# Performance work log

Measured on AMD Instinct MI355X. Metric: run time of the kernel, lower is better.

Reference implementation:

```python
import jax, jax.numpy as jnp
import numpy as np

B, S, D, H = 4, 2048, 1024, 16
DH = D // H  # 64


def setup_inputs() -> dict:
    key = jax.random.key(0)
    ks = jax.random.split(key, 8)
    sc = 1.0 / np.sqrt(D)
    return {
        "hidden_states": jax.random.normal(ks[0], (B, S, D), jnp.float32),
        "attention_mask": jnp.zeros((B, 1, 1, S), jnp.float32),
        "Wq": jax.random.normal(ks[1], (D, D), jnp.float32) * sc,
        "bq": jnp.zeros((D,), jnp.float32),
        "Wk": jax.random.normal(ks[2], (D, D), jnp.float32) * sc,
        "bk": jnp.zeros((D,), jnp.float32),
        "Wv": jax.random.normal(ks[3], (D, D), jnp.float32) * sc,
        "bv": jnp.zeros((D,), jnp.float32),
    }


def _heads(x):
    # [B,S,D] -> [B,H,S,DH]
    b, s, _ = x.shape
    return x.reshape(b, s, H, DH).transpose(0, 2, 1, 3)


def reference(hidden_states, attention_mask, Wq, bq, Wk, bk, Wv, bv):
    q = _heads(hidden_states @ Wq + bq)
    k = _heads(hidden_states @ Wk + bk)
    v = _heads(hidden_states @ Wv + bv)
    scores = jnp.einsum('bhqd,bhkd->bhqk', q, k) / jnp.sqrt(jnp.float32(DH))
    scores = scores + attention_mask  # additive mask, broadcast
    probs = jax.nn.softmax(scores, axis=-1)  # dropout is identity in eval
    out = jnp.einsum('bhqk,bhkd->bhqd', probs, v)
    b, h, s, dh = out.shape
    return out.transpose(0, 2, 1, 3).reshape(b, s, h * dh)
```

## Files before the change

kernel.cpp:

```cpp
#include <hip/hip_runtime.h>
#include <hip/hip_bf16.h>
#include <cstdint>

typedef _Float16 f16;
typedef f16 f16x8 __attribute__((ext_vector_type(8)));
typedef f16 f16x4 __attribute__((ext_vector_type(4)));
typedef float f32x4 __attribute__((ext_vector_type(4)));

#define MFMA16(a, b, c) __builtin_amdgcn_mfma_f32_16x16x32_f16((a), (b), (c), 0, 0, 0)

constexpr int Bc = 4, Sc = 2048, Dc = 1024, Hc = 16, DHc = 64;

typedef __attribute__((address_space(1))) const uint32_t gbl_u32;
typedef __attribute__((address_space(3))) uint32_t lds_u32;
__device__ __forceinline__ void gld_lds16(const void* g, void* l) {
  __builtin_amdgcn_global_load_lds((gbl_u32*)g, (lds_u32*)l, 16, 0, 0);
}

__global__ __launch_bounds__(256) void cast_w_kernel(
    const float* __restrict__ Wq, const float* __restrict__ Wk,
    const float* __restrict__ Wv, f16* __restrict__ Wt) {
  __shared__ __align__(16) f16 T[64][66];
  const int z = blockIdx.z;
  const float* W = (z == 0) ? Wq : (z == 1) ? Wk : Wv;
  const int n0 = blockIdx.x * 64, k0 = blockIdx.y * 64;
  const int t = threadIdx.x;
#pragma unroll
  for (int p = 0; p < 4; p++) {
    int idx = t + p * 256;
    int r = idx >> 4, c = idx & 15;
    float4 v = *(const float4*)(W + (size_t)(k0 + r) * Dc + n0 + c * 4);
    T[r][c * 4 + 0] = (f16)v.x;
    T[r][c * 4 + 1] = (f16)v.y;
    T[r][c * 4 + 2] = (f16)v.z;
    T[r][c * 4 + 3] = (f16)v.w;
  }
  __syncthreads();
#pragma unroll
  for (int p = 0; p < 2; p++) {
    int idx = t + p * 256;
    int n = idx >> 3, c = idx & 7;
    f16x8 tmp;
#pragma unroll
    for (int j = 0; j < 8; j++) tmp[j] = T[c * 8 + j][n];
    *(f16x8*)(Wt + ((size_t)z * Dc + n0 + n) * Dc + k0 + c * 8) = tmp;
  }
}

__global__ __launch_bounds__(256) void cast_x_kernel(const float* __restrict__ X,
                                                     f16* __restrict__ X16) {
  size_t i = ((size_t)blockIdx.x * 256 + threadIdx.x) * 8;
  float4 a = *(const float4*)(X + i);
  float4 b = *(const float4*)(X + i + 4);
  f16x8 h;
  h[0] = (f16)a.x; h[1] = (f16)a.y; h[2] = (f16)a.z; h[3] = (f16)a.w;
  h[4] = (f16)b.x; h[5] = (f16)b.y; h[6] = (f16)b.z; h[7] = (f16)b.w;
  *(f16x8*)(X16 + i) = h;
}

__global__ __launch_bounds__(256) void qkv_gemm_kernel(
    const f16* __restrict__ X16, const f16* __restrict__ Wt,
    const float* __restrict__ bq, const float* __restrict__ bk,
    const float* __restrict__ bv, f16* __restrict__ Qo, f16* __restrict__ Ko,
    f16* __restrict__ Vo) {
  const int lin = blockIdx.x;
  const int xcd = lin & 7, jj = lin >> 3;
  const int bn = jj >> 3;
  const int bm = (xcd << 3) | (jj & 7);
  const int z = bn >> 3;
  const int n0 = (bn & 7) * 128;
  const int m0 = bm * 128;
  const f16* W = Wt + (size_t)bn * 128 * Dc;
  const float* bias = (z == 0) ? bq : (z == 1) ? bk : bv;

  __shared__ __align__(16) f16 Xs[128 * 32];
  __shared__ __align__(16) f16 Ws[128 * 32];

  const int t = threadIdx.x;
  const int wave = t >> 6, lane = t & 63;
  const int l16 = lane & 15, quad = lane >> 4;
  const int wm = (wave >> 1) * 64, wn = (wave & 1) * 64;

  f32x4 acc[4][4];
#pragma unroll
  for (int i = 0; i < 4; i++)
#pragma unroll
    for (int j = 0; j < 4; j++) acc[i][j] = (f32x4){0.f, 0.f, 0.f, 0.f};

  for (int k0 = 0; k0 < Dc; k0 += 32) {
#pragma unroll
    for (int p = 0; p < 2; p++) {
      int cb = p * 256 + wave * 64;
      int chunk = cb + lane;
      int row = chunk >> 2, c8 = (chunk & 3) * 8;
      gld_lds16(X16 + (size_t)(m0 + row) * Dc + k0 + c8, (f16*)Xs + (size_t)cb * 8);
      gld_lds16(W + (size_t)row * Dc + k0 + c8, (f16*)Ws + (size_t)cb * 8);
    }
    __syncthreads();

    f16x8 aF[4], bF[4];
#pragma unroll
    for (int mt = 0; mt < 4; mt++)
      aF[mt] = *(const f16x8*)(&Xs[(wm + mt * 16 + l16) * 32 + quad * 8]);
#pragma unroll
    for (int nt = 0; nt < 4; nt++)
      bF[nt] = *(const f16x8*)(&Ws[(wn + nt * 16 + l16) * 32 + quad * 8]);
#pragma unroll
    for (int mt = 0; mt < 4; mt++)
#pragma unroll
      for (int nt = 0; nt < 4; nt++)
        acc[mt][nt] = MFMA16(aF[mt], bF[nt], acc[mt][nt]);
    __syncthreads();
  }

#pragma unroll
  for (int nt = 0; nt < 4; nt++) {
    int col = n0 + wn + nt * 16 + l16;
    float bval = bias[col];
    int h = col >> 6, d = col & 63;
    if (z == 2) {
#pragma unroll
      for (int mt = 0; mt < 4; mt++) {
        int m = m0 + wm + mt * 16 + quad * 4;
        int b = m >> 11, sbase = m & 2047;
        f16x4 pk;
#pragma unroll
        for (int r = 0; r < 4; r++) pk[r] = (f16)(acc[mt][nt][r] + bval);
        *(f16x4*)(Vo + (((size_t)(b * Hc + h)) * DHc + d) * Sc + sbase) = pk;
      }
    } else {
      const float sc = (z == 0) ? 0.18033688011112042f : 1.0f;
      f16* O = (z == 0) ? Qo : Ko;
#pragma unroll
      for (int mt = 0; mt < 4; mt++) {
#pragma unroll
        for (int r = 0; r < 4; r++) {
          int m = m0 + wm + mt * 16 + quad * 4 + r;
          int b = m >> 11, s = m & 2047;
          O[(((size_t)(b * Hc + h)) * Sc + s) * DHc + d] =
              (f16)((acc[mt][nt][r] + bval) * sc);
        }
      }
    }
  }
}

__global__ __launch_bounds__(256) void flash_kernel(
    const f16* __restrict__ Q, const f16* __restrict__ K,
    const f16* __restrict__ Vt, const float* __restrict__ mask,
    float* __restrict__ out) {
  const int lin = blockIdx.x;
  const int xcd = lin & 7, jj = lin >> 3;
  const int bh = (xcd << 3) | (jj & 7);
  const int qt = jj >> 3;
  const int b = bh >> 4, h = bh & 15;
  const int t = threadIdx.x;
  const int wave = t >> 6, lane = t & 63;
  const int l16 = lane & 15, quad = lane >> 4;
  const int qbase = qt * 128 + wave * 32;

  __shared__ __align__(16) f16 Ks[2][4096];
  __shared__ __align__(16) f16 Vs[2][4096];
  __shared__ __align__(16) float Ms[2048];

  const f16* Kb = K + (size_t)bh * Sc * DHc;
  const f16* Vb = Vt + (size_t)bh * DHc * Sc;

  constexpr float L2E = 1.44269504088896340736f;

  const int qsw8 = (quad ^ ((l16 >> 1) & 3)) * 8;

  const f16* kp[2];
  const f16* vp[2];
  int ldsOff[2];
#pragma unroll
  for (int p = 0; p < 2; p++) {
    int cb = p * 256 + wave * 64;
    int i = cb + lane;
    int half = i >> 8, row = (i >> 2) & 63, q8 = i & 3;
    int q8g = q8 ^ ((row >> 1) & 3);
    int g = (row & 32) | ((row & 12) << 1) | ((row & 16) >> 2) | (row & 3);
    kp[p] = Kb + (size_t)g * DHc + half * 32 + q8g * 8;
    vp[p] = Vb + (size_t)row * Sc + half * 32 + q8g * 8;
    ldsOff[p] = cb * 8;
  }
  auto stage = [&](int buf) {
#pragma unroll
    for (int p = 0; p < 2; p++) {
      gld_lds16(kp[p], (f16*)Ks + buf * 4096 + ldsOff[p]);
      gld_lds16(vp[p], (f16*)Vs + buf * 4096 + ldsOff[p]);
      kp[p] += 64 * DHc;
      vp[p] += 64;
    }
  };

  f16x8 qa[2][2];
#pragma unroll
  for (int mt = 0; mt < 2; mt++) {
    const f16* qb = Q + ((size_t)bh * Sc + qbase + mt * 16 + l16) * DHc;
    qa[mt][0] = *(const f16x8*)(qb + quad * 8);
    qa[mt][1] = *(const f16x8*)(qb + 32 + quad * 8);
  }

  f16x8 ones;
#pragma unroll
  for (int j = 0; j < 8; j++) ones[j] = (f16)1.0f;

  stage(0);
  {
    const float* mrow = mask + (size_t)b * Sc + t * 8;
    float4 a0 = *(const float4*)(mrow);
    float4 a1 = *(const float4*)(mrow + 4);
    f32x4 m0 = (f32x4){a0.x * L2E, a0.y * L2E, a0.z * L2E, a0.w * L2E};
    f32x4 m1 = (f32x4){a1.x * L2E, a1.y * L2E, a1.z * L2E, a1.w * L2E};
    *(f32x4*)(&Ms[t * 8]) = m0;
    *(f32x4*)(&Ms[t * 8 + 4]) = m1;
  }
  __syncthreads();

  f32x4 lacc[2];
  f32x4 o[2][4];
#pragma unroll
  for (int mt = 0; mt < 2; mt++) {
    lacc[mt] = (f32x4){0.f, 0.f, 0.f, 0.f};
#pragma unroll
    for (int dt = 0; dt < 4; dt++) o[mt][dt] = (f32x4){0.f, 0.f, 0.f, 0.f};
  }

  for (int c = 0; c < 32; c++) {
    const int buf = c & 1;
    if (c < 31) stage(buf ^ 1);

    const int mb = c * 64 + quad * 8;
    f32x4 minit[4];
    minit[0] = *(const f32x4*)(&Ms[mb + 0]);
    minit[1] = *(const f32x4*)(&Ms[mb + 4]);
    minit[2] = *(const f32x4*)(&Ms[mb + 32]);
    minit[3] = *(const f32x4*)(&Ms[mb + 36]);

    f16x8 ka[4][2];
#pragma unroll
    for (int nt = 0; nt < 4; nt++) {
      int rb = (nt * 16 + l16) * 32 + qsw8;
      ka[nt][0] = *(const f16x8*)(&Ks[buf][rb]);
      ka[nt][1] = *(const f16x8*)(&Ks[buf][2048 + rb]);
    }

    f32x4 s0[4], s1[4];
#pragma unroll
    for (int nt = 0; nt < 4; nt++) {
      f32x4 a = minit[nt];
      a = MFMA16(ka[nt][0], qa[0][0], a);
      a = MFMA16(ka[nt][1], qa[0][1], a);
      s0[nt] = a;
      f32x4 a2 = minit[nt];
      a2 = MFMA16(ka[nt][0], qa[1][0], a2);
      a2 = MFMA16(ka[nt][1], qa[1][1], a2);
      s1[nt] = a2;
    }

    f16x8 pa[2][2];
#pragma unroll
    for (int blk = 0; blk < 2; blk++) {
      f16x8 p0, p1;
#pragma unroll
      for (int half = 0; half < 2; half++) {
        int nt = blk * 2 + half;
#pragma unroll
        for (int r = 0; r < 4; r++) {
          p0[half * 4 + r] = (f16)__builtin_amdgcn_exp2f(s0[nt][r]);
          p1[half * 4 + r] = (f16)__builtin_amdgcn_exp2f(s1[nt][r]);
        }
      }
      pa[0][blk] = p0;
      pa[1][blk] = p1;
    }

    lacc[0] = MFMA16(pa[0][0], ones, lacc[0]);
    lacc[0] = MFMA16(pa[0][1], ones, lacc[0]);
    lacc[1] = MFMA16(pa[1][0], ones, lacc[1]);
    lacc[1] = MFMA16(pa[1][1], ones, lacc[1]);

#pragma unroll
    for (int dt = 0; dt < 4; dt++) {
      int rb = (dt * 16 + l16) * 32 + qsw8;
      f16x8 v0 = *(const f16x8*)(&Vs[buf][rb]);
      f16x8 v1 = *(const f16x8*)(&Vs[buf][2048 + rb]);
      o[0][dt] = MFMA16(pa[0][0], v0, o[0][dt]);
      o[0][dt] = MFMA16(pa[0][1], v1, o[0][dt]);
      o[1][dt] = MFMA16(pa[1][0], v0, o[1][dt]);
      o[1][dt] = MFMA16(pa[1][1], v1, o[1][dt]);
    }

    __syncthreads();
  }

#pragma unroll
  for (int mt = 0; mt < 2; mt++) {
    float inv[4];
#pragma unroll
    for (int r = 0; r < 4; r++) inv[r] = 1.0f / lacc[mt][r];
#pragma unroll
    for (int dt = 0; dt < 4; dt++) {
      int col = h * 64 + dt * 16 + l16;
#pragma unroll
      for (int r = 0; r < 4; r++) {
        int row = qbase + mt * 16 + quad * 4 + r;
        out[((size_t)b * Sc + row) * Dc + col] = o[mt][dt][r] * inv[r];
      }
    }
  }
}

extern "C" void kernel_launch(void* const* d_in, const int* in_sizes, int n_in,
                              void* d_out, int out_size, void* d_ws,
                              size_t ws_size, hipStream_t stream) {
  (void)in_sizes; (void)n_in; (void)out_size; (void)ws_size;
  const float* hidden = (const float*)d_in[0];
  const float* mask   = (const float*)d_in[1];
  const float* Wq     = (const float*)d_in[2];
  const float* bq     = (const float*)d_in[3];
  const float* Wk     = (const float*)d_in[4];
  const float* bk     = (const float*)d_in[5];
  const float* Wv     = (const float*)d_in[6];
  const float* bv     = (const float*)d_in[7];
  float* out = (float*)d_out;

  uint8_t* w = (uint8_t*)d_ws;
  f16* Wt   = (f16*)(w);
  f16* X16  = (f16*)(w + (size_t)6 * 1024 * 1024);
  f16* Q16  = (f16*)(w + (size_t)22 * 1024 * 1024);
  f16* K16  = (f16*)(w + (size_t)38 * 1024 * 1024);
  f16* Vt16 = (f16*)(w + (size_t)54 * 1024 * 1024);

  cast_w_kernel<<<dim3(16, 16, 3), 256, 0, stream>>>(Wq, Wk, Wv, Wt);
  cast_x_kernel<<<4096, 256, 0, stream>>>(hidden, X16);
  qkv_gemm_kernel<<<dim3(1536), 256, 0, stream>>>(X16, Wt, bq, bk, bv,
                                                  Q16, K16, Vt16);
  flash_kernel<<<dim3(1024), 256, 0, stream>>>(Q16, K16, Vt16, mask, out);
}
```

Baseline: 257.3 us.

## Split QKV GEMM into QK and V kernels with K64 swizzled LDS tiles

The single QKV projection GEMM is split into a Q/K kernel and a separate V kernel, which removes the per-block z-branch in the epilogue. Both kernels raise the K step from 32 to 64 and use an XOR-swizzled LDS layout, which halves the number of barriers per K loop and avoids LDS bank conflicts. The Q/K kernel also swaps MFMA operand order so each lane holds four consecutive head-dim values, which allows vectorized f16x4 stores and float4 bias loads instead of scalar stores. The cost is twice the LDS per block, which may lower occupancy, plus one extra kernel launch.

New measurement: 264.6 us. 2.8% more time.

```diff
diff --git a/kernel.cpp b/kernel.cpp
--- a/kernel.cpp
+++ b/kernel.cpp
@@ -58,11 +58,10 @@
   *(f16x8*)(X16 + i) = h;
 }
 
-__global__ __launch_bounds__(256) void qkv_gemm_kernel(
+__global__ __launch_bounds__(256) void qk_gemm_kernel(
     const f16* __restrict__ X16, const f16* __restrict__ Wt,
     const float* __restrict__ bq, const float* __restrict__ bk,
-    const float* __restrict__ bv, f16* __restrict__ Qo, f16* __restrict__ Ko,
-    f16* __restrict__ Vo) {
+    f16* __restrict__ Qo, f16* __restrict__ Ko) {
   const int lin = blockIdx.x;
   const int xcd = lin & 7, jj = lin >> 3;
   const int bn = jj >> 3;
@@ -71,10 +70,12 @@
   const int n0 = (bn & 7) * 128;
   const int m0 = bm * 128;
   const f16* W = Wt + (size_t)bn * 128 * Dc;
-  const float* bias = (z == 0) ? bq : (z == 1) ? bk : bv;
-
-  __shared__ __align__(16) f16 Xs[128 * 32];
-  __shared__ __align__(16) f16 Ws[128 * 32];
+  const float* bias = (z == 0) ? bq : bk;
+  f16* O = (z == 0) ? Qo : Ko;
+  const float sc = (z == 0) ? 0.18033688011112042f : 1.0f;
+
+  __shared__ __align__(16) f16 Xs[128 * 64];
+  __shared__ __align__(16) f16 Ws[128 * 64];
 
   const int t = threadIdx.x;
   const int wave = t >> 6, lane = t & 63;
@@ -87,60 +88,140 @@
 #pragma unroll
     for (int j = 0; j < 4; j++) acc[i][j] = (f32x4){0.f, 0.f, 0.f, 0.f};
 
-  for (int k0 = 0; k0 < Dc; k0 += 32) {
-#pragma unroll
-    for (int p = 0; p < 2; p++) {
-      int cb = p * 256 + wave * 64;
-      int chunk = cb + lane;
-      int row = chunk >> 2, c8 = (chunk & 3) * 8;
-      gld_lds16(X16 + (size_t)(m0 + row) * Dc + k0 + c8, (f16*)Xs + (size_t)cb * 8);
-      gld_lds16(W + (size_t)row * Dc + k0 + c8, (f16*)Ws + (size_t)cb * 8);
+  for (int k0 = 0; k0 < Dc; k0 += 64) {
+#pragma unroll
+    for (int p = 0; p < 4; p++) {
+      int i = p * 256 + wave * 64 + lane;
+      int row = i >> 3, oct = i & 7;
+      int so = (oct ^ (row & 7)) * 8;
+      gld_lds16(X16 + (size_t)(m0 + row) * Dc + k0 + so, (f16*)Xs + (size_t)i * 8);
+      gld_lds16(W + (size_t)row * Dc + k0 + so, (f16*)Ws + (size_t)i * 8);
     }
     __syncthreads();
 
-    f16x8 aF[4], bF[4];
-#pragma unroll
-    for (int mt = 0; mt < 4; mt++)
-      aF[mt] = *(const f16x8*)(&Xs[(wm + mt * 16 + l16) * 32 + quad * 8]);
-#pragma unroll
-    for (int nt = 0; nt < 4; nt++)
-      bF[nt] = *(const f16x8*)(&Ws[(wn + nt * 16 + l16) * 32 + quad * 8]);
-#pragma unroll
-    for (int mt = 0; mt < 4; mt++)
+    f16x8 aF[4][2], bF[4][2];
+#pragma unroll
+    for (int mt = 0; mt < 4; mt++) {
+      int r = wm + mt * 16 + l16;
+#pragma unroll
+      for (int kk = 0; kk < 2; kk++)
+        aF[mt][kk] =
+            *(const f16x8*)(&Xs[r * 64 + (((kk * 4 + quad) ^ (r & 7)) * 8)]);
+    }
+#pragma unroll
+    for (int nt = 0; nt < 4; nt++) {
+      int r = wn + nt * 16 + l16;
+#pragma unroll
+      for (int kk = 0; kk < 2; kk++)
+        bF[nt][kk] =
+            *(const f16x8*)(&Ws[r * 64 + (((kk * 4 + quad) ^ (r & 7)) * 8)]);
+    }
+#pragma unroll
+    for (int kk = 0; kk < 2; kk++)
 #pragma unroll
       for (int nt = 0; nt < 4; nt++)
-        acc[mt][nt] = MFMA16(aF[mt], bF[nt], acc[mt][nt]);
+#pragma unroll
+        for (int mt = 0; mt < 4; mt++)
+          acc[nt][mt] = MFMA16(bF[nt][kk], aF[mt][kk], acc[nt][mt]);
+    __syncthreads();
+  }
+
+  const int h = (n0 + wn) >> 6;
+#pragma unroll
+  for (int nt = 0; nt < 4; nt++) {
+    int cb = n0 + wn + nt * 16 + quad * 4;
+    float4 bv4 = *(const float4*)(bias + cb);
+    int d0 = nt * 16 + quad * 4;
+#pragma unroll
+    for (int mt = 0; mt < 4; mt++) {
+      int m = m0 + wm + mt * 16 + l16;
+      int b = m >> 11, s = m & 2047;
+      f16x4 pk;
+      pk[0] = (f16)((acc[nt][mt][0] + bv4.x) * sc);
+      pk[1] = (f16)((acc[nt][mt][1] + bv4.y) * sc);
+      pk[2] = (f16)((acc[nt][mt][2] + bv4.z) * sc);
+      pk[3] = (f16)((acc[nt][mt][3] + bv4.w) * sc);
+      *(f16x4*)(O + (((size_t)(b * Hc + h)) * Sc + s) * DHc + d0) = pk;
+    }
+  }
+}
+
+__global__ __launch_bounds__(256) void v_gemm_kernel(
+    const f16* __restrict__ X16, const f16* __restrict__ Wt,
+    const float* __restrict__ bv, f16* __restrict__ Vo) {
+  const int lin = blockIdx.x;
+  const int xcd = lin & 7, jj = lin >> 3;
+  const int bn = jj >> 3;
+  const int bm = (xcd << 3) | (jj & 7);
+  const int n0 = bn * 128;
+  const int m0 = bm * 128;
+  const f16* W = Wt + ((size_t)2048 + bn * 128) * Dc;
+
+  __shared__ __align__(16) f16 Xs[128 * 64];
+  __shared__ __align__(16) f16 Ws[128 * 64];
+
+  const int t = threadIdx.x;
+  const int wave = t >> 6, lane = t & 63;
+  const int l16 = lane & 15, quad = lane >> 4;
+  const int wm = (wave >> 1) * 64, wn = (wave & 1) * 64;
+
+  f32x4 acc[4][4];
+#pragma unroll
+  for (int i = 0; i < 4; i++)
+#pragma unroll
+    for (int j = 0; j < 4; j++) acc[i][j] = (f32x4){0.f, 0.f, 0.f, 0.f};
+
+  for (int k0 = 0; k0 < Dc; k0 += 64) {
+#pragma unroll
+    for (int p = 0; p < 4; p++) {
+      int i = p * 256 + wave * 64 + lane;
+      int row = i >> 3, oct = i & 7;
+      int so = (oct ^ (row & 7)) * 8;
+      gld_lds16(X16 + (size_t)(m0 + row) * Dc + k0 + so, (f16*)Xs + (size_t)i * 8);
+      gld_lds16(W + (size_t)row * Dc + k0 + so, (f16*)Ws + (size_t)i * 8);
+    }
+    __syncthreads();
+
+    f16x8 aF[4][2], bF[4][2];
+#pragma unroll
+    for (int mt = 0; mt < 4; mt++) {
+      int r = wm + mt * 16 + l16;
+#pragma unroll
+      for (int kk = 0; kk < 2; kk++)
+        aF[mt][kk] =
+            *(const f16x8*)(&Xs[r * 64 + (((kk * 4 + quad) ^ (r & 7)) * 8)]);
+    }
+#pragma unroll
+    for (int nt = 0; nt < 4; nt++) {
+      int r = wn + nt * 16 + l16;
+#pragma unroll
+      for (int kk = 0; kk < 2; kk++)
+        bF[nt][kk] =
+            *(const f16x8*)(&Ws[r * 64 + (((kk * 4 + quad) ^ (r & 7)) * 8)]);
+    }
+#pragma unroll
+    for (int kk = 0; kk < 2; kk++)
+#pragma unroll
+      for (int mt = 0; mt < 4; mt++)
+#pragma unroll
+        for (int nt = 0; nt < 4; nt++)
+          acc[mt][nt] = MFMA16(aF[mt][kk], bF[nt][kk], acc[mt][nt]);
     __syncthreads();
   }
 
 #pragma unroll
   for (int nt = 0; nt < 4; nt++) {
     int col = n0 + wn + nt * 16 + l16;
-    float bval = bias[col];
+    float bval = bv[col];
     int h = col >> 6, d = col & 63;
-    if (z == 2) {
-#pragma unroll
-      for (int mt = 0; mt < 4; mt++) {
-        int m = m0 + wm + mt * 16 + quad * 4;
-        int b = m >> 11, sbase = m & 2047;
-        f16x4 pk;
-#pragma unroll
-        for (int r = 0; r < 4; r++) pk[r] = (f16)(acc[mt][nt][r] + bval);
-        *(f16x4*)(Vo + (((size_t)(b * Hc + h)) * DHc + d) * Sc + sbase) = pk;
-      }
-    } else {
-      const float sc = (z == 0) ? 0.18033688011112042f : 1.0f;
-      f16* O = (z == 0) ? Qo : Ko;
-#pragma unroll
-      for (int mt = 0; mt < 4; mt++) {
-#pragma unroll
-        for (int r = 0; r < 4; r++) {
-          int m = m0 + wm + mt * 16 + quad * 4 + r;
-          int b = m >> 11, s = m & 2047;
-          O[(((size_t)(b * Hc + h)) * Sc + s) * DHc + d] =
-              (f16)((acc[mt][nt][r] + bval) * sc);
-        }
-      }
+#pragma unroll
+    for (int mt = 0; mt < 4; mt++) {
+      int m = m0 + wm + mt * 16 + quad * 4;
+      int b = m >> 11, sbase = m & 2047;
+      f16x4 pk;
+#pragma unroll
+      for (int r = 0; r < 4; r++) pk[r] = (f16)(acc[mt][nt][r] + bval);
+      *(f16x4*)(Vo + (((size_t)(b * Hc + h)) * DHc + d) * Sc + sbase) = pk;
     }
   }
 }
@@ -335,7 +416,7 @@
 
   cast_w_kernel<<<dim3(16, 16, 3), 256, 0, stream>>>(Wq, Wk, Wv, Wt);
   cast_x_kernel<<<4096, 256, 0, stream>>>(hidden, X16);
-  qkv_gemm_kernel<<<dim3(1536), 256, 0, stream>>>(X16, Wt, bq, bk, bv,
-                                                  Q16, K16, Vt16);
+  qk_gemm_kernel<<<dim3(1024), 256, 0, stream>>>(X16, Wt, bq, bk, Q16, K16);
+  v_gemm_kernel<<<dim3(512), 256, 0, stream>>>(X16, Wt, bv, Vt16);
   flash_kernel<<<dim3(1024), 256, 0, stream>>>(Q16, K16, Vt16, mask, out);
 }
```
